# Kernel tuning notes

Hardware: AMD Instinct MI355X
Metric: run time of the kernel (lower is better)

## Reference

```python
import jax, jax.numpy as jnp
import numpy as np

HEAD_DIM = 256
NUM_HEADS = 16
NUM_KV_HEADS = 8
EPS = 1e-6
SCALING = 256 ** -0.5  # query_pre_attn_scalar
SOFTCAP = 50.0
NEG_INF = -2.3819763e38


def setup_inputs() -> dict:
    key = jax.random.key(0)
    ks = jax.random.split(key, 8)
    B, S, HID, MAXS = 1, 2048, 3072, 4096
    hidden_states = jax.random.normal(ks[0], (B, S, HID), dtype=jnp.float32)
    # RoPE tables (complex freqs_cis represented as cos/sin), base 10000
    inv_freq = 1.0 / (10000.0 ** (np.arange(0, HEAD_DIM, 2, dtype=np.float32) / HEAD_DIM))
    t = np.arange(S, dtype=np.float32)
    ang = np.outer(t, inv_freq)  # [S, D/2]
    freqs_cos = jnp.asarray(np.cos(ang), dtype=jnp.float32)
    freqs_sin = jnp.asarray(np.sin(ang), dtype=jnp.float32)
    kv_write_indices = jnp.arange(S, dtype=jnp.int32)
    k_cache = jnp.zeros((B, MAXS, NUM_KV_HEADS, HEAD_DIM), dtype=jnp.float32)
    v_cache = jnp.zeros((B, MAXS, NUM_KV_HEADS, HEAD_DIM), dtype=jnp.float32)
    # causal mask over cache slots: query i may attend cache slot j iff j <= i
    i = jnp.arange(S)[:, None]
    j = jnp.arange(MAXS)[None, :]
    mask = jnp.where(j <= i, 0.0, NEG_INF).astype(jnp.float32)[None, None]  # [1,1,S,MAXS]
    sd = 1.0 / np.sqrt(HID)
    wq = jax.random.normal(ks[1], (HID, NUM_HEADS * HEAD_DIM), dtype=jnp.float32) * sd
    wk = jax.random.normal(ks[2], (HID, NUM_KV_HEADS * HEAD_DIM), dtype=jnp.float32) * sd
    wv = jax.random.normal(ks[3], (HID, NUM_KV_HEADS * HEAD_DIM), dtype=jnp.float32) * sd
    wo = jax.random.normal(ks[4], (NUM_HEADS * HEAD_DIM, HID), dtype=jnp.float32) * (1.0 / np.sqrt(NUM_HEADS * HEAD_DIM))
    q_norm_w = jax.random.normal(ks[5], (HEAD_DIM,), dtype=jnp.float32) * 0.02
    k_norm_w = jax.random.normal(ks[6], (HEAD_DIM,), dtype=jnp.float32) * 0.02
    return dict(hidden_states=hidden_states, freqs_cos=freqs_cos, freqs_sin=freqs_sin,
                kv_write_indices=kv_write_indices, k_cache=k_cache, v_cache=v_cache,
                mask=mask, wq=wq, wk=wk, wv=wv, wo=wo, q_norm_w=q_norm_w, k_norm_w=k_norm_w)


def _rmsnorm(x, w):
    xf = x.astype(jnp.float32)
    n = xf * jax.lax.rsqrt(jnp.mean(xf * xf, axis=-1, keepdims=True) + EPS)
    return (n * (1.0 + w.astype(jnp.float32))).astype(x.dtype)


def _rope(x, cos, sin):
    # x: [B,S,H,D]; complex rotation on (first half, second half) pairs
    D2 = x.shape[-1] // 2
    xr, xi = x[..., :D2], x[..., D2:]
    cos = cos[None, :, None, :]
    sin = sin[None, :, None, :]
    return jnp.concatenate([xr * cos - xi * sin, xr * sin + xi * cos], axis=-1).astype(x.dtype)


def reference(hidden_states, freqs_cos, freqs_sin, kv_write_indices, k_cache, v_cache,
              mask, wq, wk, wv, wo, q_norm_w, k_norm_w):
    B, S, _ = hidden_states.shape
    xq = (hidden_states @ wq).reshape(B, S, NUM_HEADS, HEAD_DIM)
    xk = (hidden_states @ wk).reshape(B, S, NUM_KV_HEADS, HEAD_DIM)
    xv = (hidden_states @ wv).reshape(B, S, NUM_KV_HEADS, HEAD_DIM)
    xq = _rmsnorm(xq, q_norm_w)
    xk = _rmsnorm(xk, k_norm_w)
    xq = _rope(xq, freqs_cos, freqs_sin)
    xk = _rope(xk, freqs_cos, freqs_sin)
    # KV-cache write (index_copy_ on dim 1)
    k_cache = k_cache.at[:, kv_write_indices].set(xk)
    v_cache = v_cache.at[:, kv_write_indices].set(xv)
    rep = NUM_HEADS // NUM_KV_HEADS
    key = jnp.repeat(k_cache, rep, axis=2)    # [B,MAXS,H,D]
    value = jnp.repeat(v_cache, rep, axis=2)
    scores = jnp.einsum('bqhd,bkhd->bhqk', xq * SCALING, key)
    scores = jnp.tanh(scores / SOFTCAP) * SOFTCAP
    scores = scores + mask
    probs = jax.nn.softmax(scores.astype(jnp.float32), axis=-1).astype(xq.dtype)
    out = jnp.einsum('bhqk,bkhd->bqhd', probs, value).reshape(B, S, NUM_HEADS * HEAD_DIM)
    return out @ wo
```

## Files before the change

kernel.cpp:

```cpp
#include <hip/hip_runtime.h>
#include <hip/hip_bf16.h>

#define S_LEN 2048
#define HID   3072
#define NH    16
#define NKV   8
#define HD    256
#define EPSV  1e-6f
#define SCALING 0.0625f
#define SOFTCAP 50.0f

typedef __attribute__((ext_vector_type(8))) short bf16x8;
typedef __attribute__((ext_vector_type(4))) float f32x4;

__device__ __forceinline__ unsigned short f2bf(float f) {
  union { float f; unsigned u; } x; x.f = f;
  unsigned r = x.u + 0x7FFFu + ((x.u >> 16) & 1u);
  return (unsigned short)(r >> 16);
}

__device__ __forceinline__ void gload_lds16(const void* g, void* l) {
  __builtin_amdgcn_global_load_lds((const __attribute__((address_space(1))) void*)g,
                                   (__attribute__((address_space(3))) void*)l, 16, 0, 0);
}

__global__ __launch_bounds__(256) void conv_b(const float* __restrict__ in,
                                              unsigned short* __restrict__ out, int n) {
  int i = (blockIdx.x * 256 + threadIdx.x) * 4;
  if (i >= n) return;
  float4 v = *(const float4*)(in + i);
  ushort4 o;
  o.x = f2bf(v.x); o.y = f2bf(v.y); o.z = f2bf(v.z); o.w = f2bf(v.w);
  *(ushort4*)(out + i) = o;
}

__global__ __launch_bounds__(256) void conv_t(const float* __restrict__ W,
                                              unsigned short* __restrict__ WT,
                                              int K, int N) {
  __shared__ float tile[64][65];
  const int n0 = blockIdx.x * 64, k0 = blockIdx.y * 64;
  const int tr = threadIdx.x >> 4;
  const int tc = threadIdx.x & 15;
#pragma unroll
  for (int i = 0; i < 4; i++) {
    float4 v = *(const float4*)(W + (size_t)(k0 + tr + 16 * i) * N + n0 + tc * 4);
    tile[tr + 16 * i][tc * 4 + 0] = v.x;
    tile[tr + 16 * i][tc * 4 + 1] = v.y;
    tile[tr + 16 * i][tc * 4 + 2] = v.z;
    tile[tr + 16 * i][tc * 4 + 3] = v.w;
  }
  __syncthreads();
#pragma unroll
  for (int i = 0; i < 4; i++) {
    int nrow = tr + 16 * i;
    ushort4 o;
    o.x = f2bf(tile[tc * 4 + 0][nrow]);
    o.y = f2bf(tile[tc * 4 + 1][nrow]);
    o.z = f2bf(tile[tc * 4 + 2][nrow]);
    o.w = f2bf(tile[tc * 4 + 3][nrow]);
    *(ushort4*)(WT + (size_t)(n0 + nrow) * K + k0 + tc * 4) = o;
  }
}

__global__ __launch_bounds__(256) void tr_bf16(const unsigned short* __restrict__ in,
                                               unsigned short* __restrict__ out,
                                               int R, int C) {
  __shared__ unsigned short tile[32][33];
  int tx = threadIdx.x & 31, ty = threadIdx.x >> 5;
  int c0 = blockIdx.x * 32, r0 = blockIdx.y * 32;
#pragma unroll
  for (int j = 0; j < 4; j++)
    tile[ty + j * 8][tx] = in[(size_t)(r0 + ty + j * 8) * C + c0 + tx];
  __syncthreads();
#pragma unroll
  for (int j = 0; j < 4; j++)
    out[(size_t)(c0 + ty + j * 8) * R + r0 + tx] = tile[tx][ty + j * 8];
}

__global__ __launch_bounds__(256) void gemm_qkv(const unsigned short* __restrict__ A,
                                                const unsigned short* __restrict__ B,
                                                float* __restrict__ XQ,
                                                float* __restrict__ XK,
                                                unsigned short* __restrict__ Vb) {
  const int K = HID;
  __shared__ unsigned short As[128 * 32];
  __shared__ unsigned short Bs[128 * 32];
  const int t = threadIdx.x;
  const int w = t >> 6, l = t & 63;
  const int bid = blockIdx.y * gridDim.x + blockIdx.x;
  const int xcd = bid & 7, ii = bid >> 3;
  const int m0 = (ii & 15) * 128;
  const int n0 = (xcd * (gridDim.x >> 3) + (ii >> 4)) * 128;
  const int wr = (w >> 1) * 64, wc = (w & 1) * 64;
  const int lr = l & 15, lk = (l >> 4) * 8;
  f32x4 acc[4][4] = {};

  const int e0 = t * 8;
  const int ar0 = e0 >> 5, ac0 = e0 & 31;
  const size_t abase = (size_t)(m0 + ar0) * K + ac0;
  const size_t bbase = (size_t)(n0 + ar0) * K + ac0;

  for (int k0 = 0; k0 < K; k0 += 32) {
    gload_lds16(A + abase + k0, As + e0);
    gload_lds16(A + abase + (size_t)64 * K + k0, As + e0 + 2048);
    gload_lds16(B + bbase + k0, Bs + e0);
    gload_lds16(B + bbase + (size_t)64 * K + k0, Bs + e0 + 2048);
    __syncthreads();
    bf16x8 af[4], bfv[4];
#pragma unroll
    for (int i = 0; i < 4; i++)
      af[i] = *(const bf16x8*)(As + (wr + i * 16 + lr) * 32 + lk);
#pragma unroll
    for (int i = 0; i < 4; i++)
      bfv[i] = *(const bf16x8*)(Bs + (wc + i * 16 + lr) * 32 + lk);
#pragma unroll
    for (int i = 0; i < 4; i++)
#pragma unroll
      for (int j = 0; j < 4; j++)
        acc[i][j] = __builtin_amdgcn_mfma_f32_16x16x32_bf16(af[i], bfv[j], acc[i][j], 0, 0, 0);
    __syncthreads();
  }

  const int rq = (l >> 4) * 4;
#pragma unroll
  for (int i = 0; i < 4; i++)
#pragma unroll
    for (int j = 0; j < 4; j++) {
      int mrow = m0 + wr + i * 16 + rq;
      int ncol = n0 + wc + j * 16 + lr;
      if (ncol < 4096) {
#pragma unroll
        for (int r = 0; r < 4; r++)
          XQ[(size_t)(mrow + r) * 4096 + ncol] = acc[i][j][r];
      } else if (ncol < 6144) {
#pragma unroll
        for (int r = 0; r < 4; r++)
          XK[(size_t)(mrow + r) * 2048 + ncol - 4096] = acc[i][j][r];
      } else {
#pragma unroll
        for (int r = 0; r < 4; r++)
          Vb[(size_t)(mrow + r) * 2048 + ncol - 6144] = f2bf(acc[i][j][r]);
      }
    }
}

__global__ __launch_bounds__(256) void gemm_nt(const unsigned short* __restrict__ A,
                                               const unsigned short* __restrict__ B,
                                               float* __restrict__ Cf,
                                               int M, int N, int K) {
  __shared__ unsigned short As[128 * 32];
  __shared__ unsigned short Bs[128 * 32];
  const int t = threadIdx.x;
  const int w = t >> 6, l = t & 63;
  const int bid = blockIdx.y * gridDim.x + blockIdx.x;
  const int xcd = bid & 7, ii = bid >> 3;
  const int m0 = (ii & 15) * 128;
  const int n0 = (xcd * (gridDim.x >> 3) + (ii >> 4)) * 128;
  const int wr = (w >> 1) * 64, wc = (w & 1) * 64;
  const int lr = l & 15, lk = (l >> 4) * 8;
  f32x4 acc[4][4] = {};

  const int e0 = t * 8;
  const int ar0 = e0 >> 5, ac0 = e0 & 31;
  const size_t abase = (size_t)(m0 + ar0) * K + ac0;
  const size_t bbase = (size_t)(n0 + ar0) * K + ac0;

  for (int k0 = 0; k0 < K; k0 += 32) {
    gload_lds16(A + abase + k0, As + e0);
    gload_lds16(A + abase + (size_t)64 * K + k0, As + e0 + 2048);
    gload_lds16(B + bbase + k0, Bs + e0);
    gload_lds16(B + bbase + (size_t)64 * K + k0, Bs + e0 + 2048);
    __syncthreads();
    bf16x8 af[4], bfv[4];
#pragma unroll
    for (int i = 0; i < 4; i++)
      af[i] = *(const bf16x8*)(As + (wr + i * 16 + lr) * 32 + lk);
#pragma unroll
    for (int i = 0; i < 4; i++)
      bfv[i] = *(const bf16x8*)(Bs + (wc + i * 16 + lr) * 32 + lk);
#pragma unroll
    for (int i = 0; i < 4; i++)
#pragma unroll
      for (int j = 0; j < 4; j++)
        acc[i][j] = __builtin_amdgcn_mfma_f32_16x16x32_bf16(af[i], bfv[j], acc[i][j], 0, 0, 0);
    __syncthreads();
  }

  const int rq = (l >> 4) * 4;
#pragma unroll
  for (int i = 0; i < 4; i++)
#pragma unroll
    for (int j = 0; j < 4; j++) {
      int mrow = m0 + wr + i * 16 + rq;
      int ncol = n0 + wc + j * 16 + lr;
#pragma unroll
      for (int r = 0; r < 4; r++)
        Cf[(size_t)(mrow + r) * N + ncol] = acc[i][j][r];
    }
}

__global__ __launch_bounds__(256) void norm_rope(const float* __restrict__ x,
                                                 unsigned short* __restrict__ out,
                                                 const float* __restrict__ w,
                                                 const float* __restrict__ fc,
                                                 const float* __restrict__ fs,
                                                 int heads_per_tok, float scale) {
  __shared__ float sh[256];
  __shared__ float red[4];
  int row = blockIdx.x;
  int t = threadIdx.x;
  float v = x[(size_t)row * 256 + t];
  float ss = v * v;
#pragma unroll
  for (int off = 32; off > 0; off >>= 1) ss += __shfl_down(ss, off);
  if ((t & 63) == 0) red[t >> 6] = ss;
  __syncthreads();
  float tot = red[0] + red[1] + red[2] + red[3];
  float rn = rsqrtf(tot * (1.0f / 256.0f) + EPSV);
  sh[t] = v * rn * (1.0f + w[t]);
  __syncthreads();
  if (t < 128) {
    int s = row / heads_per_tok;
    int h = row - s * heads_per_tok;
    size_t ob = ((size_t)h * S_LEN + s) * HD;
    float xr = sh[t], xi = sh[t + 128];
    float c = fc[(size_t)s * 128 + t], sn = fs[(size_t)s * 128 + t];
    out[ob + t]       = f2bf((xr * c - xi * sn) * scale);
    out[ob + t + 128] = f2bf((xr * sn + xi * c) * scale);
  }
}

__global__ __launch_bounds__(256) void attn(const unsigned short* __restrict__ Q,
                                            const unsigned short* __restrict__ Kc,
                                            const unsigned short* __restrict__ VT,
                                            unsigned short* __restrict__ O) {
  __shared__ unsigned short Ks[2][32 * 256];
  __shared__ unsigned short Vs[2][256 * 32];
  __shared__ unsigned short Ps[4][16][40];
  const int t = threadIdx.x, w = t >> 6, l = t & 63;
  const int n = blockIdx.x;
  const int kvh = n & 7;
  const int h = kvh * 2 + ((n >> 3) & 1);
  const int qbase = (31 - (n >> 4)) * 64;
  const int lr = l & 15, g = l >> 4, lk = g * 8;
  const int wq0 = qbase + w * 16;
  const int q_own = wq0 + lr;

  const unsigned short* Qh = Q + (size_t)h * S_LEN * HD;
  const char* Khb = (const char*)(Kc + (size_t)kvh * S_LEN * HD);
  const char* Vhb = (const char*)(VT + (size_t)kvh * HD * S_LEN);

  bf16x8 qf[8];
#pragma unroll
  for (int c = 0; c < 8; c++)
    qf[c] = *(const bf16x8*)(Qh + (size_t)(wq0 + lr) * HD + c * 32 + lk);

  f32x4 o_acc[16] = {};
  float m_s = -1e30f, l_s = 0.f;

  auto stage = [&](int kv0, int b) {
#pragma unroll
    for (int i = 0; i < 4; i++) {
      int L = t * 16 + i * 4096;
      int ks = L ^ (((L >> 9) & 7) << 4);
      gload_lds16(Khb + (size_t)kv0 * 512 + ks, (char*)(Ks[b]) + L);
    }
#pragma unroll
    for (int i = 0; i < 4; i++) {
      int L = t * 16 + i * 4096;
      int d = L >> 6;
      int kb = (L & 63) ^ (((d >> 1) & 3) << 4);
      gload_lds16(Vhb + (size_t)d * (S_LEN * 2) + (size_t)kv0 * 2 + kb, (char*)(Vs[b]) + L);
    }
  };

  const int ntB = (qbase + 64) >> 5;
  stage(0, 0);
  __syncthreads();
  int buf = 0;
  for (int tile = 0; tile < ntB; tile++) {
    const int kv0 = tile << 5;
    if (tile + 1 < ntB) stage(kv0 + 32, buf ^ 1);

    if (kv0 <= wq0 + 15) {
      const bool masked = (kv0 + 31 > wq0);
      const char* Kb = (const char*)(Ks[buf]);
      const char* Vb = (const char*)(Vs[buf]);

      f32x4 sacc[2] = {};
#pragma unroll
      for (int c = 0; c < 8; c++) {
        int a0 = (lr * 512 + c * 64 + g * 16) ^ ((lr & 7) << 4);
        bf16x8 k0f = *(const bf16x8*)(Kb + a0);
        bf16x8 k1f = *(const bf16x8*)(Kb + a0 + 8192);
        sacc[0] = __builtin_amdgcn_mfma_f32_16x16x32_bf16(k0f, qf[c], sacc[0], 0, 0, 0);
        sacc[1] = __builtin_amdgcn_mfma_f32_16x16x32_bf16(k1f, qf[c], sacc[1], 0, 0, 0);
      }

      float sv[8];
#pragma unroll
      for (int nb = 0; nb < 2; nb++)
#pragma unroll
        for (int r = 0; r < 4; r++) {
          float s = sacc[nb][r];
          float ax = fabsf(s) * (2.0f / SOFTCAP);
          float e2 = __expf(-ax);
          s = copysignf((1.f - e2) / (1.f + e2) * SOFTCAP, s);
          if (masked) {
            int kj = kv0 + nb * 16 + 4 * g + r;
            s = (kj <= q_own) ? s : -1e30f;
          }
          sv[nb * 4 + r] = s;
        }

      float mx = fmaxf(fmaxf(fmaxf(sv[0], sv[1]), fmaxf(sv[2], sv[3])),
                       fmaxf(fmaxf(sv[4], sv[5]), fmaxf(sv[6], sv[7])));
      mx = fmaxf(mx, __shfl_xor(mx, 16));
      mx = fmaxf(mx, __shfl_xor(mx, 32));
      float mnew = fmaxf(m_s, mx);
      float corr = __expf(m_s - mnew);

      float ps[8];
      float rs = 0.f;
#pragma unroll
      for (int i = 0; i < 8; i++) {
        ps[i] = __expf(sv[i] - mnew);
        rs += ps[i];
      }
      rs += __shfl_xor(rs, 16);
      rs += __shfl_xor(rs, 32);
      l_s = l_s * corr + rs;
      m_s = mnew;

      if (__any(corr < 1.0f)) {
        f32x4 c4;
#pragma unroll
        for (int r = 0; r < 4; r++) c4[r] = __shfl(corr, 4 * g + r);
#pragma unroll
        for (int fn = 0; fn < 16; fn++) o_acc[fn] *= c4;
      }

      uint2 lo, hi;
      lo.x = (unsigned)f2bf(ps[0]) | ((unsigned)f2bf(ps[1]) << 16);
      lo.y = (unsigned)f2bf(ps[2]) | ((unsigned)f2bf(ps[3]) << 16);
      hi.x = (unsigned)f2bf(ps[4]) | ((unsigned)f2bf(ps[5]) << 16);
      hi.y = (unsigned)f2bf(ps[6]) | ((unsigned)f2bf(ps[7]) << 16);
      *(uint2*)(&Ps[w][lr][4 * g])      = lo;
      *(uint2*)(&Ps[w][lr][16 + 4 * g]) = hi;

      bf16x8 pa = *(const bf16x8*)(&Ps[w][lr][8 * g]);
#pragma unroll
      for (int fn = 0; fn < 16; fn++) {
        int row = fn * 16 + lr;
        int av = (row * 64 + g * 16) ^ (((row >> 1) & 3) << 4);
        bf16x8 vf = *(const bf16x8*)(Vb + av);
        o_acc[fn] = __builtin_amdgcn_mfma_f32_16x16x32_bf16(pa, vf, o_acc[fn], 0, 0, 0);
      }
    }
    __syncthreads();
    buf ^= 1;
  }

  float inv = (l_s > 0.f) ? 1.0f / l_s : 0.f;
  f32x4 inv4;
#pragma unroll
  for (int r = 0; r < 4; r++) inv4[r] = __shfl(inv, 4 * g + r);
#pragma unroll
  for (int fn = 0; fn < 16; fn++) {
    f32x4 ov = o_acc[fn] * inv4;
#pragma unroll
    for (int r = 0; r < 4; r++) {
      int q = wq0 + g * 4 + r;
      O[(size_t)q * 4096 + h * HD + fn * 16 + lr] = f2bf(ov[r]);
    }
  }
}

extern "C" void kernel_launch(void* const* d_in, const int* in_sizes, int n_in,
                              void* d_out, int out_size, void* d_ws, size_t ws_size,
                              hipStream_t stream) {
  const float* hidden = (const float*)d_in[0];
  const float* fc  = (const float*)d_in[1];
  const float* fs  = (const float*)d_in[2];
  const float* wq  = (const float*)d_in[7];
  const float* wk  = (const float*)d_in[8];
  const float* wv  = (const float*)d_in[9];
  const float* wo  = (const float*)d_in[10];
  const float* qnw = (const float*)d_in[11];
  const float* knw = (const float*)d_in[12];
  float* out = (float*)d_out;

  char* ws = (char*)d_ws;
  size_t off = 0;
  auto alloc = [&](size_t bytes) {
    char* p = ws + off;
    off += (bytes + 255) & ~(size_t)255;
    return p;
  };
  unsigned short* Xbf    = (unsigned short*)alloc((size_t)S_LEN * HID * 2);
  unsigned short* WqkvT  = (unsigned short*)alloc((size_t)8192 * HID * 2);
  unsigned short* WoT    = (unsigned short*)alloc((size_t)HID * 4096 * 2);
  float*          XQ32   = (float*)alloc((size_t)S_LEN * 4096 * 4);
  float*          XK32   = (float*)alloc((size_t)S_LEN * 2048 * 4);
  unsigned short* Qbf    = (unsigned short*)alloc((size_t)S_LEN * 4096 * 2);
  unsigned short* Kbf    = (unsigned short*)alloc((size_t)S_LEN * 2048 * 2);
  unsigned short* Vbf    = (unsigned short*)alloc((size_t)S_LEN * 2048 * 2);
  unsigned short* Obf = (unsigned short*)XQ32;
  unsigned short* VTb = (unsigned short*)XK32;

  conv_b<<<(S_LEN * HID) / 1024, 256, 0, stream>>>(hidden, Xbf, S_LEN * HID);
  conv_t<<<dim3(4096 / 64, HID / 64), 256, 0, stream>>>(wq, WqkvT, HID, 4096);
  conv_t<<<dim3(2048 / 64, HID / 64), 256, 0, stream>>>(wk, WqkvT + (size_t)4096 * HID, HID, 2048);
  conv_t<<<dim3(2048 / 64, HID / 64), 256, 0, stream>>>(wv, WqkvT + (size_t)6144 * HID, HID, 2048);
  conv_t<<<dim3(HID / 64, 4096 / 64), 256, 0, stream>>>(wo, WoT, 4096, HID);

  gemm_qkv<<<dim3(8192 / 128, S_LEN / 128), 256, 0, stream>>>(Xbf, WqkvT, XQ32, XK32, Vbf);

  norm_rope<<<S_LEN * NH, 256, 0, stream>>>(XQ32, Qbf, qnw, fc, fs, NH, SCALING);
  norm_rope<<<S_LEN * NKV, 256, 0, stream>>>(XK32, Kbf, knw, fc, fs, NKV, 1.0f);

  tr_bf16<<<dim3(2048 / 32, 2048 / 32), 256, 0, stream>>>(Vbf, VTb, S_LEN, 2048);

  attn<<<512, 256, 0, stream>>>(Qbf, Kbf, VTb, Obf);

  gemm_nt<<<dim3(HID / 128, S_LEN / 128), 256, 0, stream>>>(Obf, WoT, out, S_LEN, HID, 4096);
}
```

Before: 681.2 us.

## Restructure QKV GEMM into 256x256 tiles with double-buffered swizzled LDS

The QKV projection GEMM now uses 256x256 output tiles computed by 512 threads. Each k-step covers 64 elements, and the next k-tile is staged into a second LDS buffer while the current one is consumed. LDS addresses are XOR-swizzled to avoid bank conflicts, and MFMA sections raise wave priority. The aim is higher data reuse, fewer barriers and load latency hidden behind compute, at the cost of 128KB of dynamic LDS and heavy register use, which restrict occupancy to one block per CU.

Measured after the change: 624.1 us. 8.4% less time.

```diff
diff --git a/kernel.cpp b/kernel.cpp
--- a/kernel.cpp
+++ b/kernel.cpp
@@ -77,57 +77,86 @@
     out[(size_t)(c0 + ty + j * 8) * R + r0 + tx] = tile[tx][ty + j * 8];
 }
 
-__global__ __launch_bounds__(256) void gemm_qkv(const unsigned short* __restrict__ A,
-                                                const unsigned short* __restrict__ B,
-                                                float* __restrict__ XQ,
-                                                float* __restrict__ XK,
-                                                unsigned short* __restrict__ Vb) {
+__global__ __launch_bounds__(512, 2) void gemm_qkv(const unsigned short* __restrict__ A,
+                                                   const unsigned short* __restrict__ B,
+                                                   float* __restrict__ XQ,
+                                                   float* __restrict__ XK,
+                                                   unsigned short* __restrict__ Vb) {
   const int K = HID;
-  __shared__ unsigned short As[128 * 32];
-  __shared__ unsigned short Bs[128 * 32];
+  extern __shared__ char smem[];
+  char* As0 = smem;
+  char* Bs0 = smem + 65536;
+
   const int t = threadIdx.x;
   const int w = t >> 6, l = t & 63;
-  const int bid = blockIdx.y * gridDim.x + blockIdx.x;
+  const int lr = l & 15, g = l >> 4;
+  const int wr = w >> 2, wc = w & 3;
+  const int bid = blockIdx.x;
   const int xcd = bid & 7, ii = bid >> 3;
-  const int m0 = (ii & 15) * 128;
-  const int n0 = (xcd * (gridDim.x >> 3) + (ii >> 4)) * 128;
-  const int wr = (w >> 1) * 64, wc = (w & 1) * 64;
-  const int lr = l & 15, lk = (l >> 4) * 8;
-  f32x4 acc[4][4] = {};
-
-  const int e0 = t * 8;
-  const int ar0 = e0 >> 5, ac0 = e0 & 31;
-  const size_t abase = (size_t)(m0 + ar0) * K + ac0;
-  const size_t bbase = (size_t)(n0 + ar0) * K + ac0;
-
-  for (int k0 = 0; k0 < K; k0 += 32) {
-    gload_lds16(A + abase + k0, As + e0);
-    gload_lds16(A + abase + (size_t)64 * K + k0, As + e0 + 2048);
-    gload_lds16(B + bbase + k0, Bs + e0);
-    gload_lds16(B + bbase + (size_t)64 * K + k0, Bs + e0 + 2048);
+  const int m0 = (ii & 7) * 256;
+  const int n0 = (xcd * 4 + (ii >> 3)) * 256;
+
+  const char* Ab = (const char*)A;
+  const char* Bb = (const char*)B;
+  const int rowbytes = K * 2;
+
+  f32x4 acc[8][4] = {};
+
+  auto stage = [&](int k0, int b) {
+#pragma unroll
+    for (int i = 0; i < 4; i++) {
+      int L = t * 16 + i * 8192;
+      int r = L >> 7;
+      int colB = (L & 127) ^ ((r & 7) << 4);
+      gload_lds16(Ab + (size_t)(m0 + r) * rowbytes + k0 * 2 + colB, As0 + b * 32768 + L);
+    }
+#pragma unroll
+    for (int i = 0; i < 4; i++) {
+      int L = t * 16 + i * 8192;
+      int r = L >> 7;
+      int colB = (L & 127) ^ ((r & 7) << 4);
+      gload_lds16(Bb + (size_t)(n0 + r) * rowbytes + k0 * 2 + colB, Bs0 + b * 32768 + L);
+    }
+  };
+
+  const int swz = (lr & 7) << 4;
+  const int NT = K / 64;
+  stage(0, 0);
+  for (int T = 0; T < NT; T++) {
     __syncthreads();
-    bf16x8 af[4], bfv[4];
-#pragma unroll
-    for (int i = 0; i < 4; i++)
-      af[i] = *(const bf16x8*)(As + (wr + i * 16 + lr) * 32 + lk);
-#pragma unroll
-    for (int i = 0; i < 4; i++)
-      bfv[i] = *(const bf16x8*)(Bs + (wc + i * 16 + lr) * 32 + lk);
-#pragma unroll
-    for (int i = 0; i < 4; i++)
-#pragma unroll
-      for (int j = 0; j < 4; j++)
-        acc[i][j] = __builtin_amdgcn_mfma_f32_16x16x32_bf16(af[i], bfv[j], acc[i][j], 0, 0, 0);
-    __syncthreads();
-  }
-
-  const int rq = (l >> 4) * 4;
-#pragma unroll
-  for (int i = 0; i < 4; i++)
+    if (T + 1 < NT) stage((T + 1) * 64, (T + 1) & 1);
+    const char* Ap = As0 + (T & 1) * 32768;
+    const char* Bp = Bs0 + (T & 1) * 32768;
+#pragma unroll
+    for (int ks = 0; ks < 2; ks++) {
+      bf16x8 af[8], bfv[4];
+#pragma unroll
+      for (int i = 0; i < 8; i++) {
+        int row = wr * 128 + i * 16 + lr;
+        af[i] = *(const bf16x8*)(Ap + ((row * 128 + ks * 64 + g * 16) ^ swz));
+      }
+#pragma unroll
+      for (int j = 0; j < 4; j++) {
+        int row = wc * 64 + j * 16 + lr;
+        bfv[j] = *(const bf16x8*)(Bp + ((row * 128 + ks * 64 + g * 16) ^ swz));
+      }
+      __builtin_amdgcn_s_setprio(1);
+#pragma unroll
+      for (int i = 0; i < 8; i++)
+#pragma unroll
+        for (int j = 0; j < 4; j++)
+          acc[i][j] = __builtin_amdgcn_mfma_f32_16x16x32_bf16(af[i], bfv[j], acc[i][j], 0, 0, 0);
+      __builtin_amdgcn_s_setprio(0);
+    }
+  }
+
+  const int rq = g * 4;
+#pragma unroll
+  for (int i = 0; i < 8; i++)
 #pragma unroll
     for (int j = 0; j < 4; j++) {
-      int mrow = m0 + wr + i * 16 + rq;
-      int ncol = n0 + wc + j * 16 + lr;
+      int mrow = m0 + wr * 128 + i * 16 + rq;
+      int ncol = n0 + wc * 64 + j * 16 + lr;
       if (ncol < 4096) {
 #pragma unroll
         for (int r = 0; r < 4; r++)
@@ -414,7 +443,7 @@
   conv_t<<<dim3(2048 / 64, HID / 64), 256, 0, stream>>>(wv, WqkvT + (size_t)6144 * HID, HID, 2048);
   conv_t<<<dim3(HID / 64, 4096 / 64), 256, 0, stream>>>(wo, WoT, 4096, HID);
 
-  gemm_qkv<<<dim3(8192 / 128, S_LEN / 128), 256, 0, stream>>>(Xbf, WqkvT, XQ32, XK32, Vbf);
+  gemm_qkv<<<256, 512, 131072, stream>>>(Xbf, WqkvT, XQ32, XK32, Vbf);
 
   norm_rope<<<S_LEN * NH, 256, 0, stream>>>(XQ32, Qbf, qnw, fc, fs, NH, SCALING);
   norm_rope<<<S_LEN * NKV, 256, 0, stream>>>(XK32, Kbf, knw, fc, fs, NKV, 1.0f);
```
